# Optimization experiments

Measured on AMD Instinct MI355X. Metric: run time of the kernel, lower is better.

## Reference

```python
import jax, jax.numpy as jnp
import numpy as np

N_NODES = 100000
N_EDGES = 1250000
NFEAT = 64
NHID = 64


def setup_inputs() -> dict:
    key = jax.random.key(0)
    k1, k2, k3 = jax.random.split(key, 3)
    x = jax.random.normal(k1, (N_NODES, NFEAT), dtype=jnp.float32)
    edge_index = jax.random.randint(k2, (2, N_EDGES), 0, N_NODES, dtype=jnp.int64)
    # Glorot-style init for the GCNConv weight [out, in]
    scale = 1.0 / np.sqrt(NFEAT)
    weight = jax.random.normal(k3, (NHID, NFEAT), dtype=jnp.float32) * scale
    bias = jnp.zeros((NHID,), dtype=jnp.float32)
    return {"x": x, "edge_index": edge_index, "weight": weight, "bias": bias}


def reference(x, edge_index, weight, bias):
    """Single-layer GCNConv: out = D^-1/2 (A+I) D^-1/2 (x W^T) + b."""
    n = x.shape[0]
    # add self-loops
    loop = jnp.arange(n, dtype=edge_index.dtype)
    src = jnp.concatenate([edge_index[0], loop])  # [E+N]
    dst = jnp.concatenate([edge_index[1], loop])
    # linear transform first (cheaper: nfeat -> nhid)
    h = x @ weight.T  # [N, nhid]
    # symmetric normalization with unit edge weights
    ones = jnp.ones_like(dst, dtype=h.dtype)
    deg = jax.ops.segment_sum(ones, dst, num_segments=n)  # [N]
    dinv = jnp.where(deg > 0, jax.lax.rsqrt(jnp.maximum(deg, 1e-12)), 0.0)
    norm = dinv[src] * dinv[dst]  # [E+N]
    # gather -> scale -> scatter-add
    msg = h[src] * norm[:, None]  # [E+N, nhid]
    out = jax.ops.segment_sum(msg, dst, num_segments=n)  # [N, nhid]
    return out + bias
```

## Files before the change

### kernel.cpp

```cpp
#include <hip/hip_runtime.h>
#include <hip/hip_fp16.h>
#include <stdint.h>

#define NF 64

#if defined(__has_builtin)
#  if __has_builtin(__builtin_amdgcn_fdot2)
#    define HAS_FDOT2 1
#  endif
#endif

typedef _Float16 half2v __attribute__((ext_vector_type(2)));
union H2 { int i; half2v v; __half2 h; float2 f_unused; };

__global__ __launch_bounds__(256) void k_ell(const int* __restrict__ src,
                                             const int* __restrict__ dst,
                                             int* degc, int* ocnt, int* oflow, int ocap,
                                             int* ell, int e, int n) {
    int grp = blockIdx.x & 7;
    int chunk = (n + 7) >> 3;
    int lo = grp * chunk;
    int hi = min(lo + chunk, n);
    int nb = gridDim.x >> 3;
    int bi = blockIdx.x >> 3;
    for (int i = bi * 256 + threadIdx.x; i < e; i += nb * 256) {
        int d = dst[i];
        if (d < lo || d >= hi) continue;
        int s = src[i];
        int slot = atomicAdd(&degc[d], 1);
        if (slot < NF) {
            ell[(unsigned)d * NF + slot] = s;
        } else {
            int o = atomicAdd(ocnt, 1);
            if (o < ocap) { oflow[2 * o] = s; oflow[2 * o + 1] = d; }
        }
    }
}

__global__ __launch_bounds__(256) void k_scale(const float* __restrict__ x,
                                               const int* __restrict__ degc,
                                               __half* __restrict__ xh, int n) {
    int i = blockIdx.x * 256 + threadIdx.x;
    int total = (n + 1) * (NF / 4);
    if (i >= total) return;
    int row = i >> 4;
    uint2 u = {0u, 0u};
    if (row < n) {
        float dd = rsqrtf((float)(degc[row] + 1));
        float4 v = reinterpret_cast<const float4*>(x)[i];
        __half2 p0 = __floats2half2_rn(v.x * dd, v.y * dd);
        __half2 p1 = __floats2half2_rn(v.z * dd, v.w * dd);
        u.x = *reinterpret_cast<unsigned*>(&p0);
        u.y = *reinterpret_cast<unsigned*>(&p1);
    }
    reinterpret_cast<uint2*>(xh)[i] = u;
}


__global__ __launch_bounds__(256) void k_agg_gemm(const __half* __restrict__ xh,
                                                  const float* __restrict__ W,
                                                  const float* __restrict__ bias,
                                                  const int* __restrict__ degc,
                                                  float* out, int n) {
    unsigned lane = threadIdx.x & 63;
    int wv = threadIdx.x >> 6;
    unsigned grp = lane >> 4;
    unsigned fl  = lane & 15;
    float bj = bias[lane];

    half2v w[32];
    {
        const float4* Wr = reinterpret_cast<const float4*>(W + (unsigned)lane * NF);
#pragma unroll
        for (int c = 0; c < 16; ++c) {
            float4 f = Wr[c];
            H2 u0; u0.h = __floats2half2_rn(f.x, f.y); w[2 * c] = u0.v;
            H2 u1; u1.h = __floats2half2_rn(f.z, f.w); w[2 * c + 1] = u1.v;
        }
    }

    const int* outi = (const int*)out;
    int ngroups = (n + 3) >> 2, gs = gridDim.x;
    int g = blockIdx.x;
    int d = g * 4 + wv;
    int ev = 0, mc = 0;
    if (d < n) {
        ev = outi[(unsigned)d * NF + lane];
        mc = degc[d];
    }
    while (g < ngroups) {
        int gn = g + gs, dn = gn * 4 + wv;
        int evn = 0, mcn = 0;
        if (gn < ngroups && dn < n) {
            evn = outi[(unsigned)dn * NF + lane];
            mcn = degc[dn];
        }
        if (d < n) {
            float dd = rsqrtf((float)(mc + 1));
            int m = min(mc, NF);
            float a0 = 0.f, a1 = 0.f, a2 = 0.f, a3 = 0.f;
            float b0 = 0.f, b1 = 0.f, b2 = 0.f, b3 = 0.f;
            float c0 = 0.f, c1 = 0.f, c2 = 0.f, c3 = 0.f;
            float e0 = 0.f, e1 = 0.f, e2 = 0.f, e3 = 0.f;
            for (int j = 0; j < m; j += 16) {
                int i0 = j + (int)grp, i1 = j + 4 + (int)grp;
                int i2 = j + 8 + (int)grp, i3 = j + 12 + (int)grp;
                int s0 = __shfl(ev, i0); s0 = (i0 < m) ? s0 : n;
                int s1 = __shfl(ev, i1); s1 = (i1 < m) ? s1 : n;
                int s2 = __shfl(ev, i2); s2 = (i2 < m) ? s2 : n;
                int s3 = __shfl(ev, i3); s3 = (i3 < m) ? s3 : n;
                uint2 u0 = *reinterpret_cast<const uint2*>(xh + (unsigned)s0 * NF + fl * 4);
                uint2 u1 = *reinterpret_cast<const uint2*>(xh + (unsigned)s1 * NF + fl * 4);
                uint2 u2 = *reinterpret_cast<const uint2*>(xh + (unsigned)s2 * NF + fl * 4);
                uint2 u3 = *reinterpret_cast<const uint2*>(xh + (unsigned)s3 * NF + fl * 4);
                float2 f;
                f = __half22float2(*reinterpret_cast<const __half2*>(&u0.x)); a0 += f.x; a1 += f.y;
                f = __half22float2(*reinterpret_cast<const __half2*>(&u0.y)); a2 += f.x; a3 += f.y;
                f = __half22float2(*reinterpret_cast<const __half2*>(&u1.x)); b0 += f.x; b1 += f.y;
                f = __half22float2(*reinterpret_cast<const __half2*>(&u1.y)); b2 += f.x; b3 += f.y;
                f = __half22float2(*reinterpret_cast<const __half2*>(&u2.x)); c0 += f.x; c1 += f.y;
                f = __half22float2(*reinterpret_cast<const __half2*>(&u2.y)); c2 += f.x; c3 += f.y;
                f = __half22float2(*reinterpret_cast<const __half2*>(&u3.x)); e0 += f.x; e1 += f.y;
                f = __half22float2(*reinterpret_cast<const __half2*>(&u3.y)); e2 += f.x; e3 += f.y;
            }
            uint2 us = *reinterpret_cast<const uint2*>(xh + (unsigned)d * NF + fl * 4);
            float2 fs0 = __half22float2(*reinterpret_cast<const __half2*>(&us.x));
            float2 fs1 = __half22float2(*reinterpret_cast<const __half2*>(&us.y));
            a0 = (a0 + b0) + (c0 + e0);
            a1 = (a1 + b1) + (c1 + e1);
            a2 = (a2 + b2) + (c2 + e2);
            a3 = (a3 + b3) + (c3 + e3);
            a0 += __shfl_xor(a0, 16); a1 += __shfl_xor(a1, 16);
            a2 += __shfl_xor(a2, 16); a3 += __shfl_xor(a3, 16);
            a0 += __shfl_xor(a0, 32); a1 += __shfl_xor(a1, 32);
            a2 += __shfl_xor(a2, 32); a3 += __shfl_xor(a3, 32);
            H2 hv0, hv1;
            hv0.h = __floats2half2_rn(dd * (a0 + fs0.x), dd * (a1 + fs0.y));
            hv1.h = __floats2half2_rn(dd * (a2 + fs1.x), dd * (a3 + fs1.y));
            int iv0 = hv0.i, iv1 = hv1.i;
            float r = bj;
#pragma unroll
            for (int c = 0; c < 16; ++c) {
                H2 p0, p1;
                p0.i = __shfl(iv0, c);
                p1.i = __shfl(iv1, c);
#ifdef HAS_FDOT2
                r = __builtin_amdgcn_fdot2(p0.v, w[2 * c], r, false);
                r = __builtin_amdgcn_fdot2(p1.v, w[2 * c + 1], r, false);
#else
                {
                    float2 av = __half22float2(p0.h);
                    H2 wb0; wb0.v = w[2 * c];
                    float2 bv = __half22float2(wb0.h);
                    r = fmaf(av.x, bv.x, r); r = fmaf(av.y, bv.y, r);
                    av = __half22float2(p1.h);
                    H2 wb1; wb1.v = w[2 * c + 1];
                    bv = __half22float2(wb1.h);
                    r = fmaf(av.x, bv.x, r); r = fmaf(av.y, bv.y, r);
                }
#endif
            }
            out[(unsigned)d * NF + lane] = r;
        }
        g = gn; d = dn; ev = evn; mc = mcn;
    }
}

__global__ __launch_bounds__(64) void k_oflow(const float* __restrict__ x,
                                              const float* __restrict__ W,
                                              const int* __restrict__ degc,
                                              const int* __restrict__ ocnt,
                                              const int* __restrict__ oflow, int ocap,
                                              float* out) {
    int c = *ocnt; if (c > ocap) c = ocap;
    int lane = threadIdx.x;
    for (int o = blockIdx.x; o < c; o += gridDim.x) {
        int s = oflow[2 * o], d = oflow[2 * o + 1];
        float norm = rsqrtf((float)(degc[s] + 1)) * rsqrtf((float)(degc[d] + 1));
        float r = 0.f;
        for (int k = 0; k < NF; ++k)
            r = fmaf(x[(long)s * NF + k], W[lane * NF + k], r);
        atomicAdd(&out[(long)d * NF + lane], norm * r);
    }
}


extern "C" void kernel_launch(void* const* d_in, const int* in_sizes, int n_in,
                              void* d_out, int out_size, void* d_ws, size_t ws_size,
                              hipStream_t stream) {
    const float* x    = (const float*)d_in[0];
    const int*   ei   = (const int*)d_in[1];
    const float* W    = (const float*)d_in[2];
    const float* bias = (const float*)d_in[3];
    float*       out  = (float*)d_out;

    const int n = in_sizes[0] / NF;
    const int e = in_sizes[1] / 2;
    const int* src = ei;
    const int* dst = ei + e;

    int*    degc = (int*)d_ws;
    int*    ocnt = degc + n;
    uintptr_t p = ((uintptr_t)(ocnt + 1) + 255) & ~(uintptr_t)255;
    __half* xh   = (__half*)p;
    int*    oflow = (int*)(xh + (size_t)(n + 1) * NF);
    long    rest = (long)ws_size - ((char*)oflow - (char*)d_ws);
    int     ocap = rest > 0 ? (int)(rest / 8) : 0;

    dim3 blk(256);
    hipMemsetAsync(degc, 0, (size_t)(n + 1) * sizeof(int), stream);
    k_ell  <<<2048, blk, 0, stream>>>(src, dst, degc, ocnt, oflow, ocap, (int*)out, e, n);
    int total4 = (n + 1) * (NF / 4);
    k_scale<<<(total4 + 255) / 256, blk, 0, stream>>>(x, degc, xh, n);
    k_agg_gemm<<<2048, blk, 0, stream>>>(xh, W, bias, degc, out, n);
    k_oflow<<<64, 64, 0, stream>>>(x, W, degc, ocnt, oflow, ocap, out);
}
```

Baseline: 149.9 us.

## Bucket ELL neighbors by source range into fixed segments and precompute dinv

Splits each node's ELL row into 8 segments of 8 slots keyed by source-index range, with per-segment atomic counters, and pre-fills the ELL with a sentinel. Aggregation uses 8 lanes per neighbor with 16-byte loads and iterates all segments, skipping only wave-wide empty ones. A separate kernel precomputes inverse sqrt degrees. The aim is locality of gathers by source range, at the cost of a larger memset, an extra fill pass, more loop iterations, and more overflow edges from the small per-segment capacity.

```diff
diff --git a/kernel.cpp b/kernel.cpp
--- a/kernel.cpp
+++ b/kernel.cpp
@@ -3,6 +3,9 @@
 #include <stdint.h>
 
 #define NF 64
+#define WSHIFT 14
+#define NSEG 8
+#define SEGSZ 8
 
 #if defined(__has_builtin)
 #  if __has_builtin(__builtin_amdgcn_fdot2)
@@ -11,11 +14,31 @@
 #endif
 
 typedef _Float16 half2v __attribute__((ext_vector_type(2)));
-union H2 { int i; half2v v; __half2 h; float2 f_unused; };
+union H2 { int i; half2v v; __half2 h; };
+
+__device__ __forceinline__ float dot2acc(half2v a, half2v b, float c) {
+#ifdef HAS_FDOT2
+    return __builtin_amdgcn_fdot2(a, b, c, false);
+#else
+    H2 ua; ua.v = a; H2 ub; ub.v = b;
+    float2 fa = __half22float2(ua.h);
+    float2 fb = __half22float2(ub.h);
+    c = fmaf(fa.x, fb.x, c);
+    return fmaf(fa.y, fb.y, c);
+#endif
+}
+
+__global__ __launch_bounds__(256) void k_fill(int* ell, int n) {
+    int4 s4;
+    s4.x = s4.y = s4.z = s4.w = n;
+    long total = (long)n * NF / 4;
+    for (long i = (long)blockIdx.x * 256 + threadIdx.x; i < total; i += (long)gridDim.x * 256)
+        reinterpret_cast<int4*>(ell)[i] = s4;
+}
 
 __global__ __launch_bounds__(256) void k_ell(const int* __restrict__ src,
                                              const int* __restrict__ dst,
-                                             int* degc, int* ocnt, int* oflow, int ocap,
+                                             int* cnt8, int* ocnt, int* oflow, int ocap,
                                              int* ell, int e, int n) {
     int grp = blockIdx.x & 7;
     int chunk = (n + 7) >> 3;
@@ -27,9 +50,10 @@
         int d = dst[i];
         if (d < lo || d >= hi) continue;
         int s = src[i];
-        int slot = atomicAdd(&degc[d], 1);
-        if (slot < NF) {
-            ell[(unsigned)d * NF + slot] = s;
+        int w = min(s >> WSHIFT, NSEG - 1);
+        int slot = atomicAdd(&cnt8[(d << 3) + w], 1);
+        if (slot < SEGSZ) {
+            ell[(unsigned)d * NF + (w << 3) + slot] = s;
         } else {
             int o = atomicAdd(ocnt, 1);
             if (o < ocap) { oflow[2 * o] = s; oflow[2 * o + 1] = d; }
@@ -37,8 +61,18 @@
     }
 }
 
+__global__ __launch_bounds__(256) void k_dinv(const int* __restrict__ cnt8,
+                                              float* __restrict__ dinv, int n) {
+    int i = blockIdx.x * 256 + threadIdx.x;
+    if (i >= n) return;
+    int4 c0 = reinterpret_cast<const int4*>(cnt8)[i * 2];
+    int4 c1 = reinterpret_cast<const int4*>(cnt8)[i * 2 + 1];
+    int deg = c0.x + c0.y + c0.z + c0.w + c1.x + c1.y + c1.z + c1.w;
+    dinv[i] = rsqrtf((float)(deg + 1));
+}
+
 __global__ __launch_bounds__(256) void k_scale(const float* __restrict__ x,
-                                               const int* __restrict__ degc,
+                                               const float* __restrict__ dinv,
                                                __half* __restrict__ xh, int n) {
     int i = blockIdx.x * 256 + threadIdx.x;
     int total = (n + 1) * (NF / 4);
@@ -46,7 +80,7 @@
     int row = i >> 4;
     uint2 u = {0u, 0u};
     if (row < n) {
-        float dd = rsqrtf((float)(degc[row] + 1));
+        float dd = dinv[row];
         float4 v = reinterpret_cast<const float4*>(x)[i];
         __half2 p0 = __floats2half2_rn(v.x * dd, v.y * dd);
         __half2 p1 = __floats2half2_rn(v.z * dd, v.w * dd);
@@ -60,12 +94,12 @@
 __global__ __launch_bounds__(256) void k_agg_gemm(const __half* __restrict__ xh,
                                                   const float* __restrict__ W,
                                                   const float* __restrict__ bias,
-                                                  const int* __restrict__ degc,
+                                                  const float* __restrict__ dinv,
                                                   float* out, int n) {
     unsigned lane = threadIdx.x & 63;
     int wv = threadIdx.x >> 6;
-    unsigned grp = lane >> 4;
-    unsigned fl  = lane & 15;
+    unsigned grp = lane >> 3;
+    unsigned fl  = lane & 7;
     float bj = bias[lane];
 
     half2v w[32];
@@ -83,92 +117,68 @@
     int ngroups = (n + 3) >> 2, gs = gridDim.x;
     int g = blockIdx.x;
     int d = g * 4 + wv;
-    int ev = 0, mc = 0;
+    int ev = 0; float dd = 0.f;
     if (d < n) {
         ev = outi[(unsigned)d * NF + lane];
-        mc = degc[d];
+        dd = dinv[d];
     }
     while (g < ngroups) {
         int gn = g + gs, dn = gn * 4 + wv;
-        int evn = 0, mcn = 0;
+        int evn = 0; float ddn = 0.f;
         if (gn < ngroups && dn < n) {
             evn = outi[(unsigned)dn * NF + lane];
-            mcn = degc[dn];
+            ddn = dinv[dn];
         }
         if (d < n) {
-            float dd = rsqrtf((float)(mc + 1));
-            int m = min(mc, NF);
             float a0 = 0.f, a1 = 0.f, a2 = 0.f, a3 = 0.f;
-            float b0 = 0.f, b1 = 0.f, b2 = 0.f, b3 = 0.f;
-            float c0 = 0.f, c1 = 0.f, c2 = 0.f, c3 = 0.f;
-            float e0 = 0.f, e1 = 0.f, e2 = 0.f, e3 = 0.f;
-            for (int j = 0; j < m; j += 16) {
-                int i0 = j + (int)grp, i1 = j + 4 + (int)grp;
-                int i2 = j + 8 + (int)grp, i3 = j + 12 + (int)grp;
-                int s0 = __shfl(ev, i0); s0 = (i0 < m) ? s0 : n;
-                int s1 = __shfl(ev, i1); s1 = (i1 < m) ? s1 : n;
-                int s2 = __shfl(ev, i2); s2 = (i2 < m) ? s2 : n;
-                int s3 = __shfl(ev, i3); s3 = (i3 < m) ? s3 : n;
-                uint2 u0 = *reinterpret_cast<const uint2*>(xh + (unsigned)s0 * NF + fl * 4);
-                uint2 u1 = *reinterpret_cast<const uint2*>(xh + (unsigned)s1 * NF + fl * 4);
-                uint2 u2 = *reinterpret_cast<const uint2*>(xh + (unsigned)s2 * NF + fl * 4);
-                uint2 u3 = *reinterpret_cast<const uint2*>(xh + (unsigned)s3 * NF + fl * 4);
+            float a4 = 0.f, a5 = 0.f, a6 = 0.f, a7 = 0.f;
+#pragma unroll
+            for (int seg = 0; seg < NSEG; ++seg) {
+                int s = __shfl(ev, (seg << 3) + (int)grp);
+                if (__all(s == n)) continue;
+                uint4 u = *reinterpret_cast<const uint4*>(xh + (unsigned)s * NF + fl * 8);
                 float2 f;
-                f = __half22float2(*reinterpret_cast<const __half2*>(&u0.x)); a0 += f.x; a1 += f.y;
-                f = __half22float2(*reinterpret_cast<const __half2*>(&u0.y)); a2 += f.x; a3 += f.y;
-                f = __half22float2(*reinterpret_cast<const __half2*>(&u1.x)); b0 += f.x; b1 += f.y;
-                f = __half22float2(*reinterpret_cast<const __half2*>(&u1.y)); b2 += f.x; b3 += f.y;
-                f = __half22float2(*reinterpret_cast<const __half2*>(&u2.x)); c0 += f.x; c1 += f.y;
-                f = __half22float2(*reinterpret_cast<const __half2*>(&u2.y)); c2 += f.x; c3 += f.y;
-                f = __half22float2(*reinterpret_cast<const __half2*>(&u3.x)); e0 += f.x; e1 += f.y;
-                f = __half22float2(*reinterpret_cast<const __half2*>(&u3.y)); e2 += f.x; e3 += f.y;
+                f = __half22float2(*reinterpret_cast<const __half2*>(&u.x)); a0 += f.x; a1 += f.y;
+                f = __half22float2(*reinterpret_cast<const __half2*>(&u.y)); a2 += f.x; a3 += f.y;
+                f = __half22float2(*reinterpret_cast<const __half2*>(&u.z)); a4 += f.x; a5 += f.y;
+                f = __half22float2(*reinterpret_cast<const __half2*>(&u.w)); a6 += f.x; a7 += f.y;
             }
-            uint2 us = *reinterpret_cast<const uint2*>(xh + (unsigned)d * NF + fl * 4);
-            float2 fs0 = __half22float2(*reinterpret_cast<const __half2*>(&us.x));
-            float2 fs1 = __half22float2(*reinterpret_cast<const __half2*>(&us.y));
-            a0 = (a0 + b0) + (c0 + e0);
-            a1 = (a1 + b1) + (c1 + e1);
-            a2 = (a2 + b2) + (c2 + e2);
-            a3 = (a3 + b3) + (c3 + e3);
-            a0 += __shfl_xor(a0, 16); a1 += __shfl_xor(a1, 16);
-            a2 += __shfl_xor(a2, 16); a3 += __shfl_xor(a3, 16);
-            a0 += __shfl_xor(a0, 32); a1 += __shfl_xor(a1, 32);
-            a2 += __shfl_xor(a2, 32); a3 += __shfl_xor(a3, 32);
-            H2 hv0, hv1;
-            hv0.h = __floats2half2_rn(dd * (a0 + fs0.x), dd * (a1 + fs0.y));
-            hv1.h = __floats2half2_rn(dd * (a2 + fs1.x), dd * (a3 + fs1.y));
-            int iv0 = hv0.i, iv1 = hv1.i;
+#pragma unroll
+            for (int mask = 8; mask <= 32; mask <<= 1) {
+                a0 += __shfl_xor(a0, mask); a1 += __shfl_xor(a1, mask);
+                a2 += __shfl_xor(a2, mask); a3 += __shfl_xor(a3, mask);
+                a4 += __shfl_xor(a4, mask); a5 += __shfl_xor(a5, mask);
+                a6 += __shfl_xor(a6, mask); a7 += __shfl_xor(a7, mask);
+            }
+            uint4 us = *reinterpret_cast<const uint4*>(xh + (unsigned)d * NF + fl * 8);
+            float2 f0 = __half22float2(*reinterpret_cast<const __half2*>(&us.x));
+            float2 f1 = __half22float2(*reinterpret_cast<const __half2*>(&us.y));
+            float2 f2 = __half22float2(*reinterpret_cast<const __half2*>(&us.z));
+            float2 f3 = __half22float2(*reinterpret_cast<const __half2*>(&us.w));
+            H2 hv0, hv1, hv2, hv3;
+            hv0.h = __floats2half2_rn(dd * (a0 + f0.x), dd * (a1 + f0.y));
+            hv1.h = __floats2half2_rn(dd * (a2 + f1.x), dd * (a3 + f1.y));
+            hv2.h = __floats2half2_rn(dd * (a4 + f2.x), dd * (a5 + f2.y));
+            hv3.h = __floats2half2_rn(dd * (a6 + f3.x), dd * (a7 + f3.y));
+            int iv0 = hv0.i, iv1 = hv1.i, iv2 = hv2.i, iv3 = hv3.i;
             float r = bj;
-#pragma unroll
-            for (int c = 0; c < 16; ++c) {
-                H2 p0, p1;
-                p0.i = __shfl(iv0, c);
-                p1.i = __shfl(iv1, c);
-#ifdef HAS_FDOT2
-                r = __builtin_amdgcn_fdot2(p0.v, w[2 * c], r, false);
-                r = __builtin_amdgcn_fdot2(p1.v, w[2 * c + 1], r, false);
-#else
-                {
-                    float2 av = __half22float2(p0.h);
-                    H2 wb0; wb0.v = w[2 * c];
-                    float2 bv = __half22float2(wb0.h);
-                    r = fmaf(av.x, bv.x, r); r = fmaf(av.y, bv.y, r);
-                    av = __half22float2(p1.h);
-                    H2 wb1; wb1.v = w[2 * c + 1];
-                    bv = __half22float2(wb1.h);
-                    r = fmaf(av.x, bv.x, r); r = fmaf(av.y, bv.y, r);
-                }
-#endif
+            H2 p;
+#pragma unroll
+            for (int f = 0; f < 8; ++f) {
+                p.i = __shfl(iv0, f); r = dot2acc(p.v, w[4 * f + 0], r);
+                p.i = __shfl(iv1, f); r = dot2acc(p.v, w[4 * f + 1], r);
+                p.i = __shfl(iv2, f); r = dot2acc(p.v, w[4 * f + 2], r);
+                p.i = __shfl(iv3, f); r = dot2acc(p.v, w[4 * f + 3], r);
             }
             out[(unsigned)d * NF + lane] = r;
         }
-        g = gn; d = dn; ev = evn; mc = mcn;
+        g = gn; d = dn; ev = evn; dd = ddn;
     }
 }
 
 __global__ __launch_bounds__(64) void k_oflow(const float* __restrict__ x,
                                               const float* __restrict__ W,
-                                              const int* __restrict__ degc,
+                                              const float* __restrict__ dinv,
                                               const int* __restrict__ ocnt,
                                               const int* __restrict__ oflow, int ocap,
                                               float* out) {
@@ -176,7 +186,7 @@
     int lane = threadIdx.x;
     for (int o = blockIdx.x; o < c; o += gridDim.x) {
         int s = oflow[2 * o], d = oflow[2 * o + 1];
-        float norm = rsqrtf((float)(degc[s] + 1)) * rsqrtf((float)(degc[d] + 1));
+        float norm = dinv[s] * dinv[d];
         float r = 0.f;
         for (int k = 0; k < NF; ++k)
             r = fmaf(x[(long)s * NF + k], W[lane * NF + k], r);
@@ -199,19 +209,22 @@
     const int* src = ei;
     const int* dst = ei + e;
 
-    int*    degc = (int*)d_ws;
-    int*    ocnt = degc + n;
-    uintptr_t p = ((uintptr_t)(ocnt + 1) + 255) & ~(uintptr_t)255;
+    int*    cnt8 = (int*)d_ws;
+    int*    ocnt = cnt8 + (size_t)n * 8;
+    float*  dinv = (float*)(ocnt + 1);
+    uintptr_t p = ((uintptr_t)(dinv + n) + 255) & ~(uintptr_t)255;
     __half* xh   = (__half*)p;
     int*    oflow = (int*)(xh + (size_t)(n + 1) * NF);
     long    rest = (long)ws_size - ((char*)oflow - (char*)d_ws);
     int     ocap = rest > 0 ? (int)(rest / 8) : 0;
 
     dim3 blk(256);
-    hipMemsetAsync(degc, 0, (size_t)(n + 1) * sizeof(int), stream);
-    k_ell  <<<2048, blk, 0, stream>>>(src, dst, degc, ocnt, oflow, ocap, (int*)out, e, n);
+    (void)hipMemsetAsync(cnt8, 0, ((size_t)n * 8 + 1) * sizeof(int), stream);
+    k_fill <<<2048, blk, 0, stream>>>((int*)out, n);
+    k_ell  <<<2048, blk, 0, stream>>>(src, dst, cnt8, ocnt, oflow, ocap, (int*)out, e, n);
+    k_dinv <<<(n + 255) / 256, blk, 0, stream>>>(cnt8, dinv, n);
     int total4 = (n + 1) * (NF / 4);
-    k_scale<<<(total4 + 255) / 256, blk, 0, stream>>>(x, degc, xh, n);
-    k_agg_gemm<<<2048, blk, 0, stream>>>(xh, W, bias, degc, out, n);
-    k_oflow<<<64, 64, 0, stream>>>(x, W, degc, ocnt, oflow, ocap, out);
-}
+    k_scale<<<(total4 + 255) / 256, blk, 0, stream>>>(x, dinv, xh, n);
+    k_agg_gemm<<<2048, blk, 0, stream>>>(xh, W, bias, dinv, out, n);
+    k_oflow<<<64, 64, 0, stream>>>(x, W, dinv, ocnt, oflow, ocap, out);
+}
```

Result: slower. 199.6 us (+33.2%).
